# Kernel optimization log

Measured on AMD Instinct MI355X. Metric: run time of the kernel, lower is better.

The kernel has to match this reference:

```python
import jax, jax.numpy as jnp
import numpy as np


def setup_inputs() -> dict:
    key = jax.random.key(0)
    x = jax.random.normal(key, (8192, 512), dtype=jnp.float32)
    return {"x": x}


def reference(x):
    n = x.shape[0]
    sq = jnp.sum(x * x, axis=1)                      # [N] squared L2 norms
    # pairwise squared distances: ||xi||^2 + ||xj||^2 - 2 xi.xj
    dist = -2.0 * (x @ x.T) + sq[None, :] + sq[:, None]  # [N, N]
    mask = jnp.triu(jnp.ones((n, n), dtype=bool), k=1)   # strict upper triangle
    # torch: norm = max row L2 norm, detached (.data)
    norm = jax.lax.stop_gradient(jnp.sqrt(jnp.max(sq)))
    count = n * (n - 1) // 2
    loss = jnp.sum(jnp.where(mask, dist, 0.0)) / (norm * count)
    return loss
```

## Files before the change

kernel.cpp:

```cpp
#include <hip/hip_runtime.h>


#define NROWS 8192
#define NCOLS 512
#define NB1   256
#define NB2   64
#define PS    (NB1 * NCOLS)
#define PM    (PS + NB1)
#define PQ    (PM + NB1)
#define PS2   (PQ + NB2)
#define PM2   (PS2 + NB2)

__global__ __launch_bounds__(256) void ndl_pass1(const float* __restrict__ x,
                                                 float* __restrict__ ws) {
    __shared__ float colsum[NCOLS];
    __shared__ float s_part[4];
    __shared__ float m_part[4];
    const int t    = threadIdx.x;
    const int lane = t & 63;
    const int wave = t >> 6;

    colsum[t]       = 0.f;
    colsum[t + 256] = 0.f;
    __syncthreads();

    const int row0 = blockIdx.x * 32 + wave * 8;
    const float4* xv = (const float4*)x;

    float col[8] = {0.f, 0.f, 0.f, 0.f, 0.f, 0.f, 0.f, 0.f};
    float sp = 0.f;
    float maxsq = 0.f;

    #pragma unroll
    for (int r = 0; r < 8; ++r) {
        const int row = row0 + r;
        float4 a = xv[row * 128 + lane * 2];
        float4 b = xv[row * 128 + lane * 2 + 1];
        col[0] += a.x; col[1] += a.y; col[2] += a.z; col[3] += a.w;
        col[4] += b.x; col[5] += b.y; col[6] += b.z; col[7] += b.w;
        float rsq = a.x*a.x + a.y*a.y + a.z*a.z + a.w*a.w
                  + b.x*b.x + b.y*b.y + b.z*b.z + b.w*b.w;
        sp += rsq;
        #pragma unroll
        for (int off = 1; off < 64; off <<= 1)
            rsq += __shfl_xor(rsq, off, 64);
        maxsq = fmaxf(maxsq, rsq);
    }

    const int base = lane * 8;
    #pragma unroll
    for (int k = 0; k < 8; ++k)
        atomicAdd(&colsum[base + k], col[k]);

    #pragma unroll
    for (int off = 1; off < 64; off <<= 1)
        sp += __shfl_xor(sp, off, 64);
    if (lane == 0) { s_part[wave] = sp; m_part[wave] = maxsq; }
    __syncthreads();

    float* o = ws + (size_t)blockIdx.x * NCOLS;
    o[t]       = colsum[t];
    o[t + 256] = colsum[t + 256];
    if (t == 0) {
        ws[PS + blockIdx.x] = s_part[0] + s_part[1] + s_part[2] + s_part[3];
        ws[PM + blockIdx.x] = fmaxf(fmaxf(m_part[0], m_part[1]),
                                    fmaxf(m_part[2], m_part[3]));
    }
}

__global__ __launch_bounds__(256) void ndl_pass2a(const float* __restrict__ ws_in,
                                                  float* __restrict__ ws) {
    __shared__ float wred[4 * 8];
    const int t    = threadIdx.x;
    const int lane = t & 63;
    const int wave = t >> 6;
    const int j    = blockIdx.x;
    const int c    = j * 8 + (t & 7);
    const int i    = t >> 3;

    const float* p = ws_in + (size_t)(i * 8) * NCOLS + c;
    float acc = 0.f;
    #pragma unroll
    for (int k = 0; k < 8; ++k)
        acc += p[(size_t)k * NCOLS];

    acc += __shfl_xor(acc, 8, 64);
    acc += __shfl_xor(acc, 16, 64);
    acc += __shfl_xor(acc, 32, 64);
    if (lane < 8) wred[wave * 8 + lane] = acc;
    __syncthreads();

    if (t < 8) {
        float cs = wred[t] + wred[8 + t] + wred[16 + t] + wred[24 + t];
        float q  = cs * cs;
        q += __shfl_xor(q, 1, 64);
        q += __shfl_xor(q, 2, 64);
        q += __shfl_xor(q, 4, 64);
        if (t == 0) ws[PQ + j] = q;
    }
    if (t == 0) {
        float s = 0.f, m = 0.f;
        #pragma unroll
        for (int k = 0; k < 4; ++k) {
            s += ws_in[PS + j * 4 + k];
            m  = fmaxf(m, ws_in[PM + j * 4 + k]);
        }
        ws[PS2 + j] = s;
        ws[PM2 + j] = m;
    }
}

__global__ __launch_bounds__(64) void ndl_pass2b(const float* __restrict__ ws,
                                                 float* __restrict__ out) {
    const int t = threadIdx.x;
    float qv = ws[PQ + t];
    float sv = ws[PS2 + t];
    float mv = ws[PM2 + t];
    #pragma unroll
    for (int off = 1; off < 64; off <<= 1) {
        qv += __shfl_xor(qv, off, 64);
        sv += __shfl_xor(sv, off, 64);
        mv  = fmaxf(mv, __shfl_xor(mv, off, 64));
    }
    if (t == 0) {
        double numer = (double)NROWS * (double)sv - (double)qv;
        double count = (double)NROWS * ((double)NROWS - 1.0) * 0.5;
        out[0] = (float)(numer / (sqrt((double)mv) * count));
    }
}

extern "C" void kernel_launch(void* const* d_in, const int* in_sizes, int n_in,
                              void* d_out, int out_size, void* d_ws, size_t ws_size,
                              hipStream_t stream) {
    const float* x = (const float*)d_in[0];
    float* out = (float*)d_out;
    float* ws  = (float*)d_ws;

    ndl_pass1<<<NB1, 256, 0, stream>>>(x, ws);
    ndl_pass2a<<<NB2, 256, 0, stream>>>(ws, ws);
    ndl_pass2b<<<1, 64, 0, stream>>>(ws, out);
}
```

Measured before the change: 68.43 us.

## Fuse final reduction into pass2 via atomics and widen pass1 blocks

Removes the third kernel launch: each pass2 block atomically accumulates its partial q, s and max into a workspace, and the last block to arrive, found with a ticket counter, computes the loss. Pass1 now uses 1024 threads per block with two rows per wave instead of eight, and pads the shared column-sum array to reduce bank conflicts on the atomics. The accumulators are zeroed by block 0 of pass1, which relies on stream ordering, and float atomic accumulation makes the result order-dependent.

```diff
diff --git a/kernel.cpp b/kernel.cpp
--- a/kernel.cpp
+++ b/kernel.cpp
@@ -7,69 +7,72 @@
 #define NB2   64
 #define PS    (NB1 * NCOLS)
 #define PM    (PS + NB1)
-#define PQ    (PM + NB1)
-#define PS2   (PQ + NB2)
-#define PM2   (PS2 + NB2)
+#define PACC  (PM + NB1)
 
-__global__ __launch_bounds__(256) void ndl_pass1(const float* __restrict__ x,
-                                                 float* __restrict__ ws) {
-    __shared__ float colsum[NCOLS];
-    __shared__ float s_part[4];
-    __shared__ float m_part[4];
+__global__ __launch_bounds__(1024) void ndl_pass1(const float* __restrict__ x,
+                                                  float* __restrict__ ws) {
+    __shared__ float colsum[NCOLS + NCOLS / 8];
+    __shared__ float s_part[16];
+    __shared__ float m_part[16];
     const int t    = threadIdx.x;
     const int lane = t & 63;
     const int wave = t >> 6;
 
-    colsum[t]       = 0.f;
-    colsum[t + 256] = 0.f;
+    if (t < NCOLS + NCOLS / 8) colsum[t] = 0.f;
+    if (blockIdx.x == 0 && t < 4) ws[PACC + t] = 0.f;
     __syncthreads();
 
-    const int row0 = blockIdx.x * 32 + wave * 8;
+    const int row0 = blockIdx.x * 32 + wave * 2;
     const float4* xv = (const float4*)x;
 
-    float col[8] = {0.f, 0.f, 0.f, 0.f, 0.f, 0.f, 0.f, 0.f};
-    float sp = 0.f;
-    float maxsq = 0.f;
+    float4 a0 = xv[(size_t)row0 * 128 + lane * 2];
+    float4 b0 = xv[(size_t)row0 * 128 + lane * 2 + 1];
+    float4 a1 = xv[(size_t)(row0 + 1) * 128 + lane * 2];
+    float4 b1 = xv[(size_t)(row0 + 1) * 128 + lane * 2 + 1];
+
+    float col[8];
+    col[0] = a0.x + a1.x; col[1] = a0.y + a1.y;
+    col[2] = a0.z + a1.z; col[3] = a0.w + a1.w;
+    col[4] = b0.x + b1.x; col[5] = b0.y + b1.y;
+    col[6] = b0.z + b1.z; col[7] = b0.w + b1.w;
+
+    float r0 = a0.x*a0.x + a0.y*a0.y + a0.z*a0.z + a0.w*a0.w
+             + b0.x*b0.x + b0.y*b0.y + b0.z*b0.z + b0.w*b0.w;
+    float r1 = a1.x*a1.x + a1.y*a1.y + a1.z*a1.z + a1.w*a1.w
+             + b1.x*b1.x + b1.y*b1.y + b1.z*b1.z + b1.w*b1.w;
 
     #pragma unroll
-    for (int r = 0; r < 8; ++r) {
-        const int row = row0 + r;
-        float4 a = xv[row * 128 + lane * 2];
-        float4 b = xv[row * 128 + lane * 2 + 1];
-        col[0] += a.x; col[1] += a.y; col[2] += a.z; col[3] += a.w;
-        col[4] += b.x; col[5] += b.y; col[6] += b.z; col[7] += b.w;
-        float rsq = a.x*a.x + a.y*a.y + a.z*a.z + a.w*a.w
-                  + b.x*b.x + b.y*b.y + b.z*b.z + b.w*b.w;
-        sp += rsq;
-        #pragma unroll
-        for (int off = 1; off < 64; off <<= 1)
-            rsq += __shfl_xor(rsq, off, 64);
-        maxsq = fmaxf(maxsq, rsq);
+    for (int off = 1; off < 64; off <<= 1) {
+        r0 += __shfl_xor(r0, off, 64);
+        r1 += __shfl_xor(r1, off, 64);
+    }
+    if (lane == 0) {
+        s_part[wave] = r0 + r1;
+        m_part[wave] = fmaxf(r0, r1);
     }
 
-    const int base = lane * 8;
+    const int base = lane * 9;
     #pragma unroll
     for (int k = 0; k < 8; ++k)
         atomicAdd(&colsum[base + k], col[k]);
-
-    #pragma unroll
-    for (int off = 1; off < 64; off <<= 1)
-        sp += __shfl_xor(sp, off, 64);
-    if (lane == 0) { s_part[wave] = sp; m_part[wave] = maxsq; }
     __syncthreads();
 
     float* o = ws + (size_t)blockIdx.x * NCOLS;
-    o[t]       = colsum[t];
-    o[t + 256] = colsum[t + 256];
+    if (t < NCOLS) o[t] = colsum[t + (t >> 3)];
     if (t == 0) {
-        ws[PS + blockIdx.x] = s_part[0] + s_part[1] + s_part[2] + s_part[3];
-        ws[PM + blockIdx.x] = fmaxf(fmaxf(m_part[0], m_part[1]),
-                                    fmaxf(m_part[2], m_part[3]));
+        float s = 0.f, m = 0.f;
+        #pragma unroll
+        for (int k = 0; k < 16; ++k) {
+            s += s_part[k];
+            m  = fmaxf(m, m_part[k]);
+        }
+        ws[PS + blockIdx.x] = s;
+        ws[PM + blockIdx.x] = m;
     }
 }
 
-__global__ __launch_bounds__(256) void ndl_pass2a(const float* __restrict__ ws_in,
-                                                  float* __restrict__ ws) {
+__global__ __launch_bounds__(256) void ndl_pass2(float* __restrict__ ws,
+                                                 float* __restrict__ out) {
     __shared__ float wred[4 * 8];
     const int t    = threadIdx.x;
     const int lane = t & 63;
@@ -78,7 +81,7 @@
     const int c    = j * 8 + (t & 7);
     const int i    = t >> 3;
 
-    const float* p = ws_in + (size_t)(i * 8) * NCOLS + c;
+    const float* p = ws + (size_t)(i * 8) * NCOLS + c;
     float acc = 0.f;
     #pragma unroll
     for (int k = 0; k < 8; ++k)
@@ -96,36 +99,29 @@
         q += __shfl_xor(q, 1, 64);
         q += __shfl_xor(q, 2, 64);
         q += __shfl_xor(q, 4, 64);
-        if (t == 0) ws[PQ + j] = q;
-    }
-    if (t == 0) {
-        float s = 0.f, m = 0.f;
-        #pragma unroll
-        for (int k = 0; k < 4; ++k) {
-            s += ws_in[PS + j * 4 + k];
-            m  = fmaxf(m, ws_in[PM + j * 4 + k]);
+        if (t == 0) {
+            float s = 0.f, m = 0.f;
+            #pragma unroll
+            for (int k = 0; k < 4; ++k) {
+                s += ws[PS + j * 4 + k];
+                m  = fmaxf(m, ws[PM + j * 4 + k]);
+            }
+            atomicAdd(&ws[PACC + 0], q);
+            atomicAdd(&ws[PACC + 1], s);
+            atomicMax((unsigned int*)&ws[PACC + 2], __float_as_uint(m));
+            __threadfence();
+            unsigned int old = atomicAdd((unsigned int*)&ws[PACC + 3], 1u);
+            if (old == NB2 - 1) {
+                __threadfence();
+                float qv = atomicAdd(&ws[PACC + 0], 0.f);
+                float sv = atomicAdd(&ws[PACC + 1], 0.f);
+                float mv = __uint_as_float(
+                    atomicMax((unsigned int*)&ws[PACC + 2], 0u));
+                double numer = (double)NROWS * (double)sv - (double)qv;
+                double count = (double)NROWS * ((double)NROWS - 1.0) * 0.5;
+                out[0] = (float)(numer / (sqrt((double)mv) * count));
+            }
         }
-        ws[PS2 + j] = s;
-        ws[PM2 + j] = m;
-    }
-}
-
-__global__ __launch_bounds__(64) void ndl_pass2b(const float* __restrict__ ws,
-                                                 float* __restrict__ out) {
-    const int t = threadIdx.x;
-    float qv = ws[PQ + t];
-    float sv = ws[PS2 + t];
-    float mv = ws[PM2 + t];
-    #pragma unroll
-    for (int off = 1; off < 64; off <<= 1) {
-        qv += __shfl_xor(qv, off, 64);
-        sv += __shfl_xor(sv, off, 64);
-        mv  = fmaxf(mv, __shfl_xor(mv, off, 64));
-    }
-    if (t == 0) {
-        double numer = (double)NROWS * (double)sv - (double)qv;
-        double count = (double)NROWS * ((double)NROWS - 1.0) * 0.5;
-        out[0] = (float)(numer / (sqrt((double)mv) * count));
     }
 }
 
@@ -136,7 +132,6 @@
     float* out = (float*)d_out;
     float* ws  = (float*)d_ws;
 
-    ndl_pass1<<<NB1, 256, 0, stream>>>(x, ws);
-    ndl_pass2a<<<NB2, 256, 0, stream>>>(ws, ws);
-    ndl_pass2b<<<1, 64, 0, stream>>>(ws, out);
+    ndl_pass1<<<NB1, 1024, 0, stream>>>(x, ws);
+    ndl_pass2<<<NB2, 256, 0, stream>>>(ws, out);
 }
```

Result: slower. 76.54 us (+11.8%).
